# Optimization experiments

Measured on AMD Instinct MI355X. Metric: run time of the kernel, lower is better.

The kernel has to match this reference:

```python
import jax, jax.numpy as jnp
import numpy as np

B, D, O, E, K = 4096, 1024, 1024, 16, 2


def setup_inputs() -> dict:
    key = jax.random.key(0)
    ks = jax.random.split(key, 3)
    x = jax.random.normal(ks[0], (B, D), jnp.float32)
    Wr = jax.random.normal(ks[1], (E, D), jnp.float32) * (D ** -0.5)
    br = jnp.zeros((E,), jnp.float32)
    We = jax.random.normal(ks[2], (E, O, D), jnp.float32) * (D ** -0.5)
    be = jnp.zeros((E, O), jnp.float32)
    return {"x": x, "Wr": Wr, "br": br, "We": We, "be": be}


def reference(x, Wr, br, We, be):
    # Router (eval mode: no gaussian noise)
    router_logits = x @ Wr.T + br                                   # [B, E]
    topk_logits, topk_indices = jax.lax.top_k(router_logits, K)     # [B, K]

    # gate[e, b] = topk logit of expert e for sample b (0 if not selected);
    # each expert appears at most once per row of topk_indices.
    onehot = jax.nn.one_hot(topk_indices, E, dtype=x.dtype)         # [B, K, E]
    gate = jnp.einsum('bke,bk->eb', onehot, topk_logits)            # [E, B]

    # All experts over full batch (dropout identity in eval), then mask by gate.
    h = jax.nn.relu(jnp.einsum('bd,eod->ebo', x, We) + be[:, None, :])  # [E, B, O]
    weighted_outputs = h * gate[:, :, None]                         # [E, B, O]
    return weighted_outputs, router_logits, topk_indices
```

## Files before the change

kernel.cpp:

```cpp
#include <hip/hip_runtime.h>
#include <hip/hip_bf16.h>
#include <cstdint>
#include <cstddef>

#define Bdim 4096
#define Ddim 1024
#define Odim 1024
#define Edim 16
#define Kdim 2

#define BM 128
#define BN 128
#define BK 64
#define NKT (Ddim / BK)
#define MAXTILES 80

typedef __attribute__((ext_vector_type(4))) float f32x4;
typedef __attribute__((ext_vector_type(8))) short bf16x8;

static __device__ __forceinline__ short f2bf(float f) {
    unsigned int u = __builtin_bit_cast(unsigned int, f);
    u = (u + 0x7FFFu + ((u >> 16) & 1u)) >> 16;
    return (short)(unsigned short)u;
}

static __device__ __forceinline__ void gload_lds16(const void* g, void* l) {
    __builtin_amdgcn_global_load_lds(
        (const __attribute__((address_space(1))) void*)g,
        (__attribute__((address_space(3))) void*)l, 16, 0, 0);
}

__global__ __launch_bounds__(256) void prep_kernel(
    const float* __restrict__ We, short* __restrict__ web,
    int* __restrict__ ntiles)
{
    const int gid = blockIdx.x * 256 + threadIdx.x;
    if (gid == 0) *ntiles = 0;
    const int stride = gridDim.x * 256;
    for (int i = gid; i < Edim * Odim * Ddim / 8; i += stride) {
        const float4* s = (const float4*)(We + (size_t)i * 8);
        float4 lo = s[0], hi = s[1];
        bf16x8 v;
        v[0] = f2bf(lo.x); v[1] = f2bf(lo.y); v[2] = f2bf(lo.z); v[3] = f2bf(lo.w);
        v[4] = f2bf(hi.x); v[5] = f2bf(hi.y); v[6] = f2bf(hi.z); v[7] = f2bf(hi.w);
        *(bf16x8*)(web + (size_t)i * 8) = v;
    }
}

__global__ __launch_bounds__(256) void router_kernel(
    const float* __restrict__ x, const float* __restrict__ Wr,
    const float* __restrict__ br,
    float* __restrict__ out_logits, float* __restrict__ out_idx,
    unsigned int* __restrict__ sel, float2* __restrict__ vals,
    short* __restrict__ xb)
{
    const int wave = threadIdx.x >> 6;
    const int lane = threadIdx.x & 63;
    const int b = blockIdx.x * 4 + wave;
    const int e = lane >> 2;
    const int q = lane & 3;

    const float4* xr = (const float4*)(x + (size_t)b * Ddim + q * 256);
    const float4* wr = (const float4*)(Wr + (size_t)e * Ddim + q * 256);
    double acc = 0.0;
#pragma unroll 8
    for (int i = 0; i < 64; ++i) {
        float4 xv = xr[i], wv = wr[i];
        acc += (double)xv.x * (double)wv.x;
        acc += (double)xv.y * (double)wv.y;
        acc += (double)xv.z * (double)wv.z;
        acc += (double)xv.w * (double)wv.w;
    }
    acc += __shfl_xor(acc, 1);
    acc += __shfl_xor(acc, 2);
    float logit = (float)acc + br[e];
    float v = __shfl(logit, (lane & 15) * 4);

    if (lane < Edim) out_logits[(size_t)b * Edim + lane] = v;

    const float4* xr4 = (const float4*)(x + (size_t)b * Ddim);
#pragma unroll
    for (int it = 0; it < 2; ++it) {
        int off = (it * 64 + lane) * 2;
        float4 lo = xr4[off], hi = xr4[off + 1];
        bf16x8 vv;
        vv[0] = f2bf(lo.x); vv[1] = f2bf(lo.y); vv[2] = f2bf(lo.z); vv[3] = f2bf(lo.w);
        vv[4] = f2bf(hi.x); vv[5] = f2bf(hi.y); vv[6] = f2bf(hi.z); vv[7] = f2bf(hi.w);
        *(bf16x8*)(xb + (size_t)b * Ddim + off * 4) = vv;
    }

    float v1 = v; int i1 = lane & 15;
#pragma unroll
    for (int m = 1; m < 16; m <<= 1) {
        float ov = __shfl_xor(v1, m);
        int   oi = __shfl_xor(i1, m);
        if (ov > v1 || (ov == v1 && oi < i1)) { v1 = ov; i1 = oi; }
    }
    float vc = ((lane & 15) == i1) ? -INFINITY : v;
    float v2 = vc; int i2 = lane & 15;
#pragma unroll
    for (int m = 1; m < 16; m <<= 1) {
        float ov = __shfl_xor(v2, m);
        int   oi = __shfl_xor(i2, m);
        if (ov > v2 || (ov == v2 && oi < i2)) { v2 = ov; i2 = oi; }
    }

    if (lane == 0) {
        out_idx[(size_t)b * Kdim + 0] = (float)i1;
        out_idx[(size_t)b * Kdim + 1] = (float)i2;
        sel[b]  = (unsigned int)i1 | ((unsigned int)i2 << 8);
        vals[b] = make_float2(v1, v2);
    }
}

__global__ __launch_bounds__(256) void compact_kernel(
    const unsigned int* __restrict__ sel, const float2* __restrict__ vals,
    int* __restrict__ counts, int* __restrict__ rowids, float* __restrict__ gates,
    int* __restrict__ ntiles, int* __restrict__ desc)
{
    const int e = blockIdx.x;
    const int tid = threadIdx.x;
    const int lane = tid & 63;
    const int w = tid >> 6;
    __shared__ int wcnt[4];

    int base = 0;
    for (int c = 0; c < Bdim; c += 256) {
        int b = c + tid;
        unsigned int s = sel[b];
        int e1 = s & 0xff, e2 = (s >> 8) & 0xff;
        bool f = (e1 == e) || (e2 == e);
        float2 vv = vals[b];
        float g = (e1 == e) ? vv.x : vv.y;
        unsigned long long m = __ballot(f);
        int my = __popcll(m & ((1ULL << lane) - 1ULL));
        if (lane == 0) wcnt[w] = __popcll(m);
        __syncthreads();
        int wbase = 0;
#pragma unroll
        for (int i = 0; i < 4; ++i) wbase += (i < w) ? wcnt[i] : 0;
        int tot = wcnt[0] + wcnt[1] + wcnt[2] + wcnt[3];
        if (f) {
            int p = base + wbase + my;
            rowids[e * Bdim + p] = b;
            gates [e * Bdim + p] = g;
        }
        base += tot;
        __syncthreads();
    }
    if (tid == 0) {
        counts[e] = base;
        int nt = (base + BM - 1) / BM;
        int tb = atomicAdd(ntiles, nt);
        for (int i = 0; i < nt; ++i) desc[tb + i] = (e << 8) | i;
    }
}

__global__ __launch_bounds__(256) void moe_gemm(
    const short* __restrict__ xb, const short* __restrict__ web,
    const float* __restrict__ be, const int* __restrict__ counts,
    const int* __restrict__ rowids, const float* __restrict__ gates,
    const int* __restrict__ ntiles, const int* __restrict__ desc,
    float* __restrict__ out)
{
    const int bid  = blockIdx.x;
    const int tile = bid >> 3;
    const int ty   = bid & 7;
    if (tile >= *ntiles) return;
    const int d  = desc[tile];
    const int e  = d >> 8;
    const int tx = d & 255;

    const int cnt = counts[e];
    const int r0 = tx * BM;
    const int tile_rows = min(BM, cnt - r0);

    __shared__ short sA[BM * BK];
    __shared__ short sB[BN * BK];
    __shared__ int   s_row[BM];
    __shared__ float s_gate[BM];

    const int tid = threadIdx.x;
    if (tid < BM) {
        int rr = min(tid, tile_rows - 1);
        s_row[tid]  = rowids[e * Bdim + r0 + rr];
        s_gate[tid] = (tid < tile_rows) ? gates[e * Bdim + r0 + tid] : 0.0f;
    }
    __syncthreads();

    const int rA  = tid >> 3;
    const int kc2 = (tid & 7) ^ (rA & 7);
    const short* asrc[4];
    const short* bsrcp[4];
    const short* bpanel = web + ((size_t)e * Odim + ty * BN) * Ddim;
#pragma unroll
    for (int i = 0; i < 4; ++i) {
        asrc[i]  = xb + (size_t)s_row[i * 32 + rA] * Ddim + kc2 * 8;
        bsrcp[i] = bpanel + (size_t)(i * 32 + rA) * Ddim + kc2 * 8;
    }
    const int wave_elem = (tid & ~63) * 8;

    const int lane = tid & 63;
    const int wid  = tid >> 6;
    const int wm = wid >> 1, wn = wid & 1;
    const int fr = lane & 15;
    const int fq = lane >> 4;

    f32x4 acc[4][4] = {};

    for (int kt = 0; kt < NKT; ++kt) {
        const int k0 = kt * BK;
#pragma unroll
        for (int i = 0; i < 4; ++i)
            gload_lds16(asrc[i] + k0, &sA[i * 2048 + wave_elem]);
#pragma unroll
        for (int i = 0; i < 4; ++i)
            gload_lds16(bsrcp[i] + k0, &sB[i * 2048 + wave_elem]);
        __syncthreads();
#pragma unroll
        for (int kk = 0; kk < 2; ++kk) {
            bf16x8 af[4], bfr[4];
#pragma unroll
            for (int m = 0; m < 4; ++m) {
                int r = wm * 64 + m * 16 + fr;
                int sc = (kk * 4 + fq) ^ (fr & 7);
                af[m] = *(const bf16x8*)&sA[r * BK + sc * 8];
            }
#pragma unroll
            for (int n = 0; n < 4; ++n) {
                int r = wn * 64 + n * 16 + fr;
                int sc = (kk * 4 + fq) ^ (fr & 7);
                bfr[n] = *(const bf16x8*)&sB[r * BK + sc * 8];
            }
#pragma unroll
            for (int m = 0; m < 4; ++m)
#pragma unroll
                for (int n = 0; n < 4; ++n)
                    acc[m][n] = __builtin_amdgcn_mfma_f32_16x16x32_bf16(
                        af[m], bfr[n], acc[m][n], 0, 0, 0);
        }
        __syncthreads();
    }

    const size_t ebase = (size_t)e * Bdim;
    const int col0 = ty * BN + wn * 64;
#pragma unroll
    for (int m = 0; m < 4; ++m) {
        int rbase = wm * 64 + m * 16 + fq * 4;
#pragma unroll
        for (int j = 0; j < 4; ++j) {
            int r = rbase + j;
            if (r < tile_rows) {
                int brow = s_row[r];
                float g  = s_gate[r];
                float* op = out + (ebase + brow) * Odim + col0;
#pragma unroll
                for (int n = 0; n < 4; ++n) {
                    int o = n * 16 + fr;
                    float h = acc[m][n][j] + be[e * Odim + col0 + o];
                    h = fmaxf(h, 0.0f);
                    __builtin_nontemporal_store(h * g, op + o);
                }
            }
        }
    }
}

extern "C" void kernel_launch(void* const* d_in, const int* in_sizes, int n_in,
                              void* d_out, int out_size, void* d_ws, size_t ws_size,
                              hipStream_t stream)
{
    const float* x  = (const float*)d_in[0];
    const float* Wr = (const float*)d_in[1];
    const float* br = (const float*)d_in[2];
    const float* We = (const float*)d_in[3];
    const float* be = (const float*)d_in[4];

    float* out_w      = (float*)d_out;
    float* out_logits = out_w + (size_t)Edim * Bdim * Odim;
    float* out_idx    = out_logits + (size_t)Bdim * Edim;

    char* w = (char*)d_ws;
    int*          counts = (int*)w;
    int*          ntiles = (int*)(w + 64);
    int*          desc   = (int*)(w + 128);
    unsigned int* sel    = (unsigned int*)(w + 512);
    float2*       vals   = (float2*)(w + 512 + 4 * Bdim);
    int*          rowids = (int*)(w + 512 + 12 * Bdim);
    float*        gates  = (float*)(w + 512 + 12 * Bdim + 4 * Edim * Bdim);
    short*        xb     = (short*)(w + 512 + 12 * Bdim + 8 * Edim * Bdim);
    short*        web    = xb + (size_t)Bdim * Ddim;

    prep_kernel<<<2048, 256, 0, stream>>>(We, web, ntiles);

    router_kernel<<<Bdim / 4, 256, 0, stream>>>(
        x, Wr, br, out_logits, out_idx, sel, vals, xb);

    compact_kernel<<<Edim, 256, 0, stream>>>(
        sel, vals, counts, rowids, gates, ntiles, desc);

    moe_gemm<<<MAXTILES * 8, 256, 0, stream>>>(
        xb, web, be, counts, rowids, gates, ntiles, desc, out_w);
}
```

Before: 120.1 us.

## Fuse expert-weight bf16 conversion into GEMM B-tile loads

Removes the separate prep kernel that converted all expert weights from fp32 to bf16. The GEMM now streams fp32 weight tiles straight into LDS with a swizzled layout and converts them to bf16 with packed convert instructions while building the MFMA fragments. This saves a full read and write pass over the 64 MB weight tensor. In exchange the GEMM reads twice as many bytes per B tile, uses more LDS, and adds conversion ALU work to the inner loop.

```diff
diff --git a/kernel.cpp b/kernel.cpp
--- a/kernel.cpp
+++ b/kernel.cpp
@@ -17,6 +17,7 @@
 
 typedef __attribute__((ext_vector_type(4))) float f32x4;
 typedef __attribute__((ext_vector_type(8))) short bf16x8;
+typedef __attribute__((ext_vector_type(4))) unsigned int u32x4;
 
 static __device__ __forceinline__ short f2bf(float f) {
     unsigned int u = __builtin_bit_cast(unsigned int, f);
@@ -28,23 +29,6 @@
     __builtin_amdgcn_global_load_lds(
         (const __attribute__((address_space(1))) void*)g,
         (__attribute__((address_space(3))) void*)l, 16, 0, 0);
-}
-
-__global__ __launch_bounds__(256) void prep_kernel(
-    const float* __restrict__ We, short* __restrict__ web,
-    int* __restrict__ ntiles)
-{
-    const int gid = blockIdx.x * 256 + threadIdx.x;
-    if (gid == 0) *ntiles = 0;
-    const int stride = gridDim.x * 256;
-    for (int i = gid; i < Edim * Odim * Ddim / 8; i += stride) {
-        const float4* s = (const float4*)(We + (size_t)i * 8);
-        float4 lo = s[0], hi = s[1];
-        bf16x8 v;
-        v[0] = f2bf(lo.x); v[1] = f2bf(lo.y); v[2] = f2bf(lo.z); v[3] = f2bf(lo.w);
-        v[4] = f2bf(hi.x); v[5] = f2bf(hi.y); v[6] = f2bf(hi.z); v[7] = f2bf(hi.w);
-        *(bf16x8*)(web + (size_t)i * 8) = v;
-    }
 }
 
 __global__ __launch_bounds__(256) void router_kernel(
@@ -52,8 +36,9 @@
     const float* __restrict__ br,
     float* __restrict__ out_logits, float* __restrict__ out_idx,
     unsigned int* __restrict__ sel, float2* __restrict__ vals,
-    short* __restrict__ xb)
+    short* __restrict__ xb, int* __restrict__ ntiles)
 {
+    if (blockIdx.x == 0 && threadIdx.x == 0) *ntiles = 0;
     const int wave = threadIdx.x >> 6;
     const int lane = threadIdx.x & 63;
     const int b = blockIdx.x * 4 + wave;
@@ -157,7 +142,7 @@
 }
 
 __global__ __launch_bounds__(256) void moe_gemm(
-    const short* __restrict__ xb, const short* __restrict__ web,
+    const short* __restrict__ xb, const float* __restrict__ We,
     const float* __restrict__ be, const int* __restrict__ counts,
     const int* __restrict__ rowids, const float* __restrict__ gates,
     const int* __restrict__ ntiles, const int* __restrict__ desc,
@@ -176,7 +161,7 @@
     const int tile_rows = min(BM, cnt - r0);
 
     __shared__ short sA[BM * BK];
-    __shared__ short sB[BN * BK];
+    __shared__ float sBf[BN * BK];
     __shared__ int   s_row[BM];
     __shared__ float s_gate[BM];
 
@@ -189,16 +174,22 @@
     __syncthreads();
 
     const int rA  = tid >> 3;
-    const int kc2 = (tid & 7) ^ (rA & 7);
+    const int kcA = (tid & 7) ^ (rA & 7);
     const short* asrc[4];
-    const short* bsrcp[4];
-    const short* bpanel = web + ((size_t)e * Odim + ty * BN) * Ddim;
-#pragma unroll
-    for (int i = 0; i < 4; ++i) {
-        asrc[i]  = xb + (size_t)s_row[i * 32 + rA] * Ddim + kc2 * 8;
-        bsrcp[i] = bpanel + (size_t)(i * 32 + rA) * Ddim + kc2 * 8;
-    }
-    const int wave_elem = (tid & ~63) * 8;
+#pragma unroll
+    for (int i = 0; i < 4; ++i)
+        asrc[i] = xb + (size_t)s_row[i * 32 + rA] * Ddim + kcA * 8;
+
+    const int rB  = tid >> 4;
+    const int kcB = (tid & 15) ^ (rB & 15);
+    const float* bpanel = We + ((size_t)e * Odim + ty * BN) * Ddim;
+    const float* bsrcf[8];
+#pragma unroll
+    for (int i = 0; i < 8; ++i)
+        bsrcf[i] = bpanel + (size_t)(i * 16 + rB) * Ddim + kcB * 4;
+
+    const int waveA = (tid & ~63) * 8;
+    const int waveB = (tid & ~63) * 4;
 
     const int lane = tid & 63;
     const int wid  = tid >> 6;
@@ -212,10 +203,10 @@
         const int k0 = kt * BK;
 #pragma unroll
         for (int i = 0; i < 4; ++i)
-            gload_lds16(asrc[i] + k0, &sA[i * 2048 + wave_elem]);
-#pragma unroll
-        for (int i = 0; i < 4; ++i)
-            gload_lds16(bsrcp[i] + k0, &sB[i * 2048 + wave_elem]);
+            gload_lds16(asrc[i] + k0, &sA[i * 2048 + waveA]);
+#pragma unroll
+        for (int i = 0; i < 8; ++i)
+            gload_lds16(bsrcf[i] + k0, &sBf[i * 1024 + waveB]);
         __syncthreads();
 #pragma unroll
         for (int kk = 0; kk < 2; ++kk) {
@@ -229,8 +220,16 @@
 #pragma unroll
             for (int n = 0; n < 4; ++n) {
                 int r = wn * 64 + n * 16 + fr;
-                int sc = (kk * 4 + fq) ^ (fr & 7);
-                bfr[n] = *(const bf16x8*)&sB[r * BK + sc * 8];
+                int q0 = kk * 8 + fq * 2;
+                f32x4 p0 = *(const f32x4*)&sBf[r * BK + ((q0    ) ^ fr) * 4];
+                f32x4 p1 = *(const f32x4*)&sBf[r * BK + ((q0 + 1) ^ fr) * 4];
+                unsigned int w0, w1, w2, w3;
+                asm("v_cvt_pk_bf16_f32 %0, %1, %2" : "=v"(w0) : "v"(p0[0]), "v"(p0[1]));
+                asm("v_cvt_pk_bf16_f32 %0, %1, %2" : "=v"(w1) : "v"(p0[2]), "v"(p0[3]));
+                asm("v_cvt_pk_bf16_f32 %0, %1, %2" : "=v"(w2) : "v"(p1[0]), "v"(p1[1]));
+                asm("v_cvt_pk_bf16_f32 %0, %1, %2" : "=v"(w3) : "v"(p1[2]), "v"(p1[3]));
+                u32x4 pk = {w0, w1, w2, w3};
+                bfr[n] = __builtin_bit_cast(bf16x8, pk);
             }
 #pragma unroll
             for (int m = 0; m < 4; ++m)
@@ -289,16 +288,13 @@
     int*          rowids = (int*)(w + 512 + 12 * Bdim);
     float*        gates  = (float*)(w + 512 + 12 * Bdim + 4 * Edim * Bdim);
     short*        xb     = (short*)(w + 512 + 12 * Bdim + 8 * Edim * Bdim);
-    short*        web    = xb + (size_t)Bdim * Ddim;
-
-    prep_kernel<<<2048, 256, 0, stream>>>(We, web, ntiles);
 
     router_kernel<<<Bdim / 4, 256, 0, stream>>>(
-        x, Wr, br, out_logits, out_idx, sel, vals, xb);
+        x, Wr, br, out_logits, out_idx, sel, vals, xb, ntiles);
 
     compact_kernel<<<Edim, 256, 0, stream>>>(
         sel, vals, counts, rowids, gates, ntiles, desc);
 
     moe_gemm<<<MAXTILES * 8, 256, 0, stream>>>(
-        xb, web, be, counts, rowids, gates, ntiles, desc, out_w);
-}
+        xb, We, be, counts, rowids, gates, ntiles, desc, out_w);
+}
```

Result: slower. 129.7 us (+8.0%).
